# Optimization experiments

Hardware: AMD Instinct MI355X
Metric: run time of the kernel (lower is better)

Reference implementation:

```python
import jax, jax.numpy as jnp
import numpy as np

N = 100000
E = 3200000
D = 128
H = 128
BN_EPS = 1e-5


def setup_inputs() -> dict:
    key = jax.random.key(0)
    ks = jax.random.split(key, 8)
    x = jax.random.normal(ks[0], (N, D), dtype=jnp.float32)
    edge_index = jax.random.randint(ks[1], (2, E), 0, N, dtype=jnp.int64)
    edge_attr = jax.random.normal(ks[2], (E, 1), dtype=jnp.float32)
    # MLP params (Linear stores weight [out,in]; we keep [in,out] for x @ W)
    W1 = jax.random.normal(ks[3], (D, H), dtype=jnp.float32) / np.sqrt(D)
    b1 = jnp.zeros((H,), dtype=jnp.float32)
    W2 = jax.random.normal(ks[4], (H, H), dtype=jnp.float32) / np.sqrt(H)
    b2 = jnp.zeros((H,), dtype=jnp.float32)
    gamma = jnp.ones((H,), dtype=jnp.float32)
    beta = jnp.zeros((H,), dtype=jnp.float32)
    return {"x": x, "edge_index": edge_index, "edge_attr": edge_attr,
            "W1": W1, "b1": b1, "W2": W2, "b2": b2,
            "gamma": gamma, "beta": beta}


def reference(x, edge_index, edge_attr, W1, b1, W2, b2, gamma, beta):
    src, dst = edge_index[0], edge_index[1]
    # GIN aggregation: (1 + eps) * x_i + sum_{j->i} x_j, eps = 0
    agg = jax.ops.segment_sum(x[src], dst, num_segments=N)  # [N, D]
    h = x + agg
    # 2-layer MLP
    h = jax.nn.relu(h @ W1 + b1)
    h = h @ W2 + b2
    # outer ReLU
    h = jax.nn.relu(h)
    # BatchNorm1d (training mode: batch stats, biased variance)
    mean = jnp.mean(h, axis=0)
    var = jnp.mean(jnp.square(h - mean), axis=0)
    h = (h - mean) * jax.lax.rsqrt(var + BN_EPS) * gamma + beta
    return h
```

## Files before the change

kernel.cpp:

```cpp
#include <hip/hip_runtime.h>

#define N_NODES 100000
#define DIM 128
#define PT_TILE 4096
#define PT_THR 512

#define NPB1 196
#define NB1 511
#define CAP1 7168
#define NPB2 256
#define NB2 391
#define CAP2 12288

typedef unsigned int u32;
typedef unsigned short u16;
typedef __attribute__((ext_vector_type(8))) short bf16x8;
typedef __attribute__((ext_vector_type(4))) float f32x4;

__device__ __forceinline__ float bf16_to_f(u16 v) {
  return __uint_as_float(((u32)v) << 16);
}
__device__ __forceinline__ u16 f_to_bf16(float f) {
  u32 b = __float_as_uint(f);
  b += 0x7fff + ((b >> 16) & 1);
  return (u16)(b >> 16);
}
__device__ __forceinline__ float blo(u32 q) { return __uint_as_float(q << 16); }
__device__ __forceinline__ float bhi(u32 q) {
  return __uint_as_float(q & 0xffff0000u);
}
__device__ __forceinline__ u32 packbf(float lo, float hi) {
  return ((u32)f_to_bf16(hi) << 16) | (u32)f_to_bf16(lo);
}

__global__ __launch_bounds__(256) void prep1_kernel(
    const float* __restrict__ W1, u16* __restrict__ Wt1,
    const float* __restrict__ W2, u16* __restrict__ Wt2,
    int* __restrict__ gcur, float* __restrict__ stats) {
  int blk = blockIdx.x;
  if (blk < 64) {
    int id = blk * 256 + threadIdx.x;
    Wt1[id] = f_to_bf16(W1[(id & 127) * DIM + (id >> 7)]);
  } else if (blk < 128) {
    int id = (blk - 64) * 256 + threadIdx.x;
    Wt2[id] = f_to_bf16(W2[(id & 127) * DIM + (id >> 7)]);
  } else if (blk == 128) {
    for (int i = threadIdx.x; i < NB1; i += 256) gcur[i] = i * CAP1;
  } else {
    for (int i = threadIdx.x; i < 768; i += 256) stats[i] = 0.f;
  }
}

__global__ __launch_bounds__(256) void prep2_kernel(
    const float* __restrict__ W1, u16* __restrict__ Wt1,
    const float* __restrict__ W2, u16* __restrict__ Wt2,
    const int* __restrict__ ei, int* __restrict__ bcnt, int E_) {
  int blk = blockIdx.x;
  if (blk < 64) {
    int id = blk * 256 + threadIdx.x;
    Wt1[id] = f_to_bf16(W1[(id & 127) * DIM + (id >> 7)]);
  } else if (blk < 128) {
    int id = (blk - 64) * 256 + threadIdx.x;
    Wt2[id] = f_to_bf16(W2[(id & 127) * DIM + (id >> 7)]);
  } else {
    __shared__ int lc[NB2];
    for (int i = threadIdx.x; i < NB2; i += 256) lc[i] = 0;
    __syncthreads();
    const int* dst = ei + E_;
    int G = 512 * 256;
    int g = (blk - 128) * 256 + threadIdx.x;
    int n4 = E_ >> 2;
    const int4* d4 = (const int4*)dst;
    for (int i = g; i < n4; i += G) {
      int4 v = d4[i];
      atomicAdd(&lc[((u32)v.x) >> 8], 1);
      atomicAdd(&lc[((u32)v.y) >> 8], 1);
      atomicAdd(&lc[((u32)v.z) >> 8], 1);
      atomicAdd(&lc[((u32)v.w) >> 8], 1);
    }
    for (int e = (n4 << 2) + g; e < E_; e += G)
      atomicAdd(&lc[((u32)dst[e]) >> 8], 1);
    __syncthreads();
    for (int i = threadIdx.x; i < NB2; i += 256)
      if (lc[i]) atomicAdd(&bcnt[i], lc[i]);
  }
}

__global__ void bscan_kernel(const int* __restrict__ bcnt,
                             int* __restrict__ boffs, int* __restrict__ gcur) {
  __shared__ int s[256];
  int t = threadIdx.x;
  int v0 = (2 * t < NB2) ? bcnt[2 * t] : 0;
  int v1 = (2 * t + 1 < NB2) ? bcnt[2 * t + 1] : 0;
  int ts = v0 + v1;
  s[t] = ts;
  __syncthreads();
  for (int o = 1; o < 256; o <<= 1) {
    int u = (t >= o) ? s[t - o] : 0;
    __syncthreads();
    s[t] += u;
    __syncthreads();
  }
  int excl = s[t] - ts;
  if (2 * t <= NB2) boffs[2 * t] = excl;
  if (2 * t + 1 <= NB2) boffs[2 * t + 1] = excl + v0;
  if (2 * t < NB2) gcur[2 * t] = excl;
  if (2 * t + 1 < NB2) gcur[2 * t + 1] = excl + v0;
}

template <int NPB, int NBU>
__global__ __launch_bounds__(PT_THR) void part_cvt_kernel(
    const int* __restrict__ ei, int* __restrict__ gcur,
    u32* __restrict__ packed, int E_, const float* __restrict__ x,
    u16* __restrict__ xb) {
  __shared__ u32 keys[PT_TILE];
  __shared__ u16 bid[PT_TILE];
  __shared__ int lh[NBU];
  __shared__ int lpos[NBU];
  __shared__ int gpos[NBU];
  __shared__ int ss[PT_THR];
  const int nPart = (E_ + PT_TILE - 1) / PT_TILE;
  const int t = threadIdx.x;

  if (blockIdx.x >= nPart) {
    int cb = blockIdx.x - nPart;
    int total = N_NODES * DIM / 4;
    int stride = 1024 * PT_THR;
    for (int i = cb * PT_THR + t; i < total; i += stride) {
      float4 v = reinterpret_cast<const float4*>(x)[i];
      ushort4 o;
      o.x = f_to_bf16(v.x);
      o.y = f_to_bf16(v.y);
      o.z = f_to_bf16(v.z);
      o.w = f_to_bf16(v.w);
      reinterpret_cast<ushort4*>(xb)[i] = o;
    }
    return;
  }

  const int base = blockIdx.x * PT_TILE;
  const int cnt = min(PT_TILE, E_ - base);

  for (int i = t; i < NBU; i += PT_THR) lh[i] = 0;
  __syncthreads();

  u32 pk[8];
  int bb[8];
#pragma unroll
  for (int k = 0; k < 8; ++k) {
    int e = base + k * PT_THR + t;
    if (k * PT_THR + t < cnt) {
      int src = ei[e];
      u32 dst = (u32)ei[E_ + e];
      u32 b = dst / NPB;
      bb[k] = (int)b;
      pk[k] = (u32)src | ((dst - b * NPB) << 17);
      atomicAdd(&lh[bb[k]], 1);
    } else {
      bb[k] = -1;
    }
  }
  __syncthreads();

  int v = (t < NBU) ? lh[t] : 0;
  ss[t] = v;
  __syncthreads();
  for (int o = 1; o < PT_THR; o <<= 1) {
    int u = (t >= o) ? ss[t - o] : 0;
    __syncthreads();
    ss[t] += u;
    __syncthreads();
  }
  if (t < NBU) {
    lpos[t] = ss[t] - v;
    if (v > 0) gpos[t] = atomicAdd(&gcur[t], v);
  }
  __syncthreads();

#pragma unroll
  for (int k = 0; k < 8; ++k) {
    if (bb[k] >= 0) {
      int p = atomicAdd(&lpos[bb[k]], 1);
      keys[p] = pk[k];
      bid[p] = (u16)bb[k];
    }
  }
  __syncthreads();

  for (int i = t; i < cnt; i += PT_THR) {
    int b = bid[i];
    int startb = lpos[b] - lh[b];
    packed[gpos[b] + (i - startb)] = keys[i];
  }
}

template <int NPB, int LCAP, bool FIXED>
__global__ __launch_bounds__(1024) void sortgather_kernel(
    const u32* __restrict__ packed, const int* __restrict__ boffs,
    const int* __restrict__ gcur, const uint4* __restrict__ xb4,
    uint4* __restrict__ hb4) {
  __shared__ u32 sorted_[LCAP];
  __shared__ int hist[256], cur[256], ssc[256];
  __shared__ int nodeoff[257];
  const int b = blockIdx.x;
  const int t = threadIdx.x;
  int base, cnt;
  if (FIXED) {
    base = b * LCAP;
    cnt = gcur[b] - base;
  } else {
    base = boffs[b];
    cnt = boffs[b + 1] - base;
  }
  if (cnt > LCAP) cnt = LCAP;
  if (cnt < 0) cnt = 0;

  if (t < 256) hist[t] = 0;
  __syncthreads();
  for (int i = t; i < cnt; i += 1024)
    atomicAdd(&hist[packed[base + i] >> 17], 1);
  __syncthreads();
  if (t < 256) ssc[t] = hist[t];
  __syncthreads();
  for (int o = 1; o < 256; o <<= 1) {
    int u = 0;
    if (t < 256 && t >= o) u = ssc[t - o];
    __syncthreads();
    if (t < 256) ssc[t] += u;
    __syncthreads();
  }
  if (t < 256) {
    int excl = ssc[t] - hist[t];
    cur[t] = excl;
    nodeoff[t] = excl;
  }
  if (t == 0) nodeoff[256] = cnt;
  __syncthreads();
  for (int i = t; i < cnt; i += 1024) {
    u32 v = packed[base + i];
    int p = atomicAdd(&cur[v >> 17], 1);
    sorted_[p] = v & 0x1FFFFu;
  }
  __syncthreads();

  const int wv = t >> 6;
  const int lane = t & 63;
  const int g = lane >> 4;
  const int l = lane & 15;
  constexpr int K = (NPB + 15) / 16;
#pragma unroll 1
  for (int k = 0; k < K; ++k) {
    int nl = wv + (k << 4);
    if (nl >= NPB) break;
    int n = b * NPB + nl;
    if (n >= N_NODES) break;
    int beg = nodeoff[nl], end = nodeoff[nl + 1];
    float a0 = 0.f, a1 = 0.f, a2 = 0.f, a3 = 0.f;
    float a4 = 0.f, a5 = 0.f, a6 = 0.f, a7 = 0.f;
    if (g == 0) {
      uint4 q = xb4[(size_t)n * 16 + l];
      a0 = blo(q.x); a1 = bhi(q.x);
      a2 = blo(q.y); a3 = bhi(q.y);
      a4 = blo(q.z); a5 = bhi(q.z);
      a6 = blo(q.w); a7 = bhi(q.w);
    }
    int j = beg + g;
    for (; j + 12 < end; j += 16) {
      int s0 = sorted_[j], s1 = sorted_[j + 4];
      int s2 = sorted_[j + 8], s3 = sorted_[j + 12];
      uint4 q0 = xb4[(size_t)s0 * 16 + l];
      uint4 q1 = xb4[(size_t)s1 * 16 + l];
      uint4 q2 = xb4[(size_t)s2 * 16 + l];
      uint4 q3 = xb4[(size_t)s3 * 16 + l];
      a0 += blo(q0.x); a1 += bhi(q0.x);
      a2 += blo(q0.y); a3 += bhi(q0.y);
      a4 += blo(q0.z); a5 += bhi(q0.z);
      a6 += blo(q0.w); a7 += bhi(q0.w);
      a0 += blo(q1.x); a1 += bhi(q1.x);
      a2 += blo(q1.y); a3 += bhi(q1.y);
      a4 += blo(q1.z); a5 += bhi(q1.z);
      a6 += blo(q1.w); a7 += bhi(q1.w);
      a0 += blo(q2.x); a1 += bhi(q2.x);
      a2 += blo(q2.y); a3 += bhi(q2.y);
      a4 += blo(q2.z); a5 += bhi(q2.z);
      a6 += blo(q2.w); a7 += bhi(q2.w);
      a0 += blo(q3.x); a1 += bhi(q3.x);
      a2 += blo(q3.y); a3 += bhi(q3.y);
      a4 += blo(q3.z); a5 += bhi(q3.z);
      a6 += blo(q3.w); a7 += bhi(q3.w);
    }
    for (; j < end; j += 4) {
      uint4 q = xb4[(size_t)sorted_[j] * 16 + l];
      a0 += blo(q.x); a1 += bhi(q.x);
      a2 += blo(q.y); a3 += bhi(q.y);
      a4 += blo(q.z); a5 += bhi(q.z);
      a6 += blo(q.w); a7 += bhi(q.w);
    }
    a0 += __shfl_xor(a0, 16); a1 += __shfl_xor(a1, 16);
    a2 += __shfl_xor(a2, 16); a3 += __shfl_xor(a3, 16);
    a4 += __shfl_xor(a4, 16); a5 += __shfl_xor(a5, 16);
    a6 += __shfl_xor(a6, 16); a7 += __shfl_xor(a7, 16);
    a0 += __shfl_xor(a0, 32); a1 += __shfl_xor(a1, 32);
    a2 += __shfl_xor(a2, 32); a3 += __shfl_xor(a3, 32);
    a4 += __shfl_xor(a4, 32); a5 += __shfl_xor(a5, 32);
    a6 += __shfl_xor(a6, 32); a7 += __shfl_xor(a7, 32);
    if (g == 0) {
      uint4 o;
      o.x = packbf(a0, a1);
      o.y = packbf(a2, a3);
      o.z = packbf(a4, a5);
      o.w = packbf(a6, a7);
      hb4[(size_t)n * 16 + l] = o;
    }
  }
}

__global__ __launch_bounds__(256) void mlp_mfma_kernel(
    u16* __restrict__ hb, const u16* __restrict__ Wt1,
    const u16* __restrict__ Wt2, const float* __restrict__ b1,
    const float* __restrict__ b2, float* __restrict__ pstats) {
  __shared__ u16 sH1[4][16 * DIM];
  __shared__ float sS[4][128], sQ[4][128];
  const int tid = threadIdx.x;
  const int wv = tid >> 6;
  const int lane = tid & 63;
  const int lr = lane & 15;
  const int lq = lane >> 4;
  const int row0 = blockIdx.x * 64 + wv * 16;

  bf16x8 a[4];
  {
    int r = row0 + lr;
    if (r > N_NODES - 1) r = N_NODES - 1;
#pragma unroll
    for (int ks = 0; ks < 4; ++ks)
      a[ks] = *reinterpret_cast<const bf16x8*>(hb + (size_t)r * DIM + ks * 32 +
                                               lq * 8);
  }
  f32x4 acc[8];
#pragma unroll
  for (int ct = 0; ct < 8; ++ct) {
    f32x4 c = {0.f, 0.f, 0.f, 0.f};
#pragma unroll
    for (int ks = 0; ks < 4; ++ks) {
      bf16x8 b = *reinterpret_cast<const bf16x8*>(
          Wt1 + (ct * 16 + lr) * DIM + ks * 32 + lq * 8);
      c = __builtin_amdgcn_mfma_f32_16x16x32_bf16(a[ks], b, c, 0, 0, 0);
    }
    acc[ct] = c;
  }
  char* slab = reinterpret_cast<char*>(&sH1[wv][0]);
#pragma unroll
  for (int ct = 0; ct < 8; ++ct) {
    int c = ct * 16 + lr;
    float bias = b1[c];
#pragma unroll
    for (int j = 0; j < 4; ++j) {
      int rl = lq * 4 + j;
      float y = fmaxf(acc[ct][j] + bias, 0.f);
      int byte = rl * 256 + ((c * 2) ^ ((rl & 7) << 4));
      *reinterpret_cast<u16*>(slab + byte) = f_to_bf16(y);
    }
  }
  __syncthreads();

  bf16x8 a2[4];
#pragma unroll
  for (int ks = 0; ks < 4; ++ks) {
    int byte = lr * 256 + (((ks * 32 + lq * 8) * 2) ^ ((lr & 7) << 4));
    a2[ks] = *reinterpret_cast<const bf16x8*>(slab + byte);
  }
#pragma unroll
  for (int ct = 0; ct < 8; ++ct) {
    f32x4 c = {0.f, 0.f, 0.f, 0.f};
#pragma unroll
    for (int ks = 0; ks < 4; ++ks) {
      bf16x8 b = *reinterpret_cast<const bf16x8*>(
          Wt2 + (ct * 16 + lr) * DIM + ks * 32 + lq * 8);
      c = __builtin_amdgcn_mfma_f32_16x16x32_bf16(a2[ks], b, c, 0, 0, 0);
    }
    acc[ct] = c;
  }
  float ls[8], lss[8];
#pragma unroll
  for (int ct = 0; ct < 8; ++ct) {
    int c = ct * 16 + lr;
    float bias = b2[c];
    ls[ct] = 0.f;
    lss[ct] = 0.f;
#pragma unroll
    for (int j = 0; j < 4; ++j) {
      int r = row0 + lq * 4 + j;
      float y = fmaxf(acc[ct][j] + bias, 0.f);
      u16 yq = f_to_bf16(y);
      float yf = bf16_to_f(yq);
      if (r < N_NODES) {
        hb[(size_t)r * DIM + c] = yq;
        ls[ct] += yf;
        lss[ct] += yf * yf;
      }
    }
  }
#pragma unroll
  for (int ct = 0; ct < 8; ++ct) {
    float s = ls[ct], q = lss[ct];
    s += __shfl_xor(s, 16);
    q += __shfl_xor(q, 16);
    s += __shfl_xor(s, 32);
    q += __shfl_xor(q, 32);
    if (lq == 0) {
      sS[wv][ct * 16 + lr] = s;
      sQ[wv][ct * 16 + lr] = q;
    }
  }
  __syncthreads();
  {
    int t = tid;
    float v;
    if (t < 128)
      v = sS[0][t] + sS[1][t] + sS[2][t] + sS[3][t];
    else
      v = sQ[0][t - 128] + sQ[1][t - 128] + sQ[2][t - 128] + sQ[3][t - 128];
    pstats[(size_t)blockIdx.x * 256 + t] = v;
  }
}

__global__ __launch_bounds__(256) void bn_reduce_kernel(
    const float* __restrict__ pstats, float* __restrict__ stats, int nblk) {
  int t = threadIdx.x;
  float v = 0.f;
  for (int i = blockIdx.x; i < nblk; i += gridDim.x)
    v += pstats[(size_t)i * 256 + t];
  atomicAdd(&stats[t], v);
}

__global__ __launch_bounds__(256) void bn_apply_bf16_kernel(
    const uint4* __restrict__ hb4, const float* __restrict__ stats,
    const float* __restrict__ gamma, const float* __restrict__ beta,
    float4* __restrict__ out4) {
  __shared__ float sSc[128], sSh[128];
  int t = threadIdx.x;
  if (t < 128) {
    float mean = stats[t] / (float)N_NODES;
    float var = stats[128 + t] / (float)N_NODES - mean * mean;
    float scale = gamma[t] * rsqrtf(var + 1e-5f);
    sSc[t] = scale;
    sSh[t] = beta[t] - mean * scale;
  }
  __syncthreads();
  int total = N_NODES * 16;
  int stride = gridDim.x * 256;
  for (int i = blockIdx.x * 256 + t; i < total; i += stride) {
    uint4 q = hb4[i];
    int cb = (i & 15) * 8;
    float4 o0, o1;
    o0.x = blo(q.x) * sSc[cb + 0] + sSh[cb + 0];
    o0.y = bhi(q.x) * sSc[cb + 1] + sSh[cb + 1];
    o0.z = blo(q.y) * sSc[cb + 2] + sSh[cb + 2];
    o0.w = bhi(q.y) * sSc[cb + 3] + sSh[cb + 3];
    o1.x = blo(q.z) * sSc[cb + 4] + sSh[cb + 4];
    o1.y = bhi(q.z) * sSc[cb + 5] + sSh[cb + 5];
    o1.z = blo(q.w) * sSc[cb + 6] + sSh[cb + 6];
    o1.w = bhi(q.w) * sSc[cb + 7] + sSh[cb + 7];
    out4[2 * i] = o0;
    out4[2 * i + 1] = o1;
  }
}

__global__ __launch_bounds__(256) void scatter_kernel(
    const float* __restrict__ x, const int* __restrict__ ei,
    float* __restrict__ h, int E_) {
  long long total = (long long)E_ * 32;
  long long stride = (long long)gridDim.x * blockDim.x;
  for (long long idx = (long long)blockIdx.x * blockDim.x + threadIdx.x;
       idx < total; idx += stride) {
    int e = (int)(idx >> 5);
    int q = (int)(idx & 31);
    float4 v =
        *reinterpret_cast<const float4*>(x + (size_t)ei[e] * DIM + q * 4);
    float* p = h + (size_t)ei[E_ + e] * DIM + q * 4;
    atomicAdd(p + 0, v.x);
    atomicAdd(p + 1, v.y);
    atomicAdd(p + 2, v.z);
    atomicAdd(p + 3, v.w);
  }
}

__global__ __launch_bounds__(256) void add_x_kernel(const float* __restrict__ x,
                                                    float* __restrict__ h) {
  size_t total = (size_t)N_NODES * DIM / 4;
  size_t stride = (size_t)gridDim.x * blockDim.x;
  for (size_t i = (size_t)blockIdx.x * blockDim.x + threadIdx.x; i < total;
       i += stride) {
    float4 v = reinterpret_cast<float4*>(h)[i];
    float4 xv = reinterpret_cast<const float4*>(x)[i];
    v.x += xv.x; v.y += xv.y; v.z += xv.z; v.w += xv.w;
    reinterpret_cast<float4*>(h)[i] = v;
  }
}

__global__ __launch_bounds__(256) void mlp_valu_kernel(
    float* hbuf, const float* __restrict__ W1, const float* __restrict__ b1,
    const float* __restrict__ W2, const float* __restrict__ b2) {
  __shared__ float sW[DIM * DIM];
  __shared__ float sH[32][DIM];
  const int tid = threadIdx.x;
  const int col = tid & 127;
  const int rhalf = tid >> 7;
  const int row0 = blockIdx.x * 32;

  for (int i = tid; i < DIM * DIM; i += 256) sW[i] = W1[i];
  for (int i = tid; i < 32 * DIM; i += 256) {
    int r = i >> 7, c = i & 127;
    sH[r][c] = hbuf[(size_t)(row0 + r) * DIM + c];
  }
  __syncthreads();
  float acc[16];
  float bias = b1[col];
#pragma unroll
  for (int j = 0; j < 16; ++j) acc[j] = bias;
#pragma unroll 4
  for (int k = 0; k < DIM; ++k) {
    float w = sW[k * DIM + col];
#pragma unroll
    for (int j = 0; j < 16; ++j) acc[j] = fmaf(sH[2 * j + rhalf][k], w, acc[j]);
  }
  __syncthreads();
  for (int i = tid; i < DIM * DIM; i += 256) sW[i] = W2[i];
#pragma unroll
  for (int j = 0; j < 16; ++j) sH[2 * j + rhalf][col] = fmaxf(acc[j], 0.f);
  __syncthreads();
  float bias2 = b2[col];
#pragma unroll
  for (int j = 0; j < 16; ++j) acc[j] = bias2;
#pragma unroll 4
  for (int k = 0; k < DIM; ++k) {
    float w = sW[k * DIM + col];
#pragma unroll
    for (int j = 0; j < 16; ++j) acc[j] = fmaf(sH[2 * j + rhalf][k], w, acc[j]);
  }
#pragma unroll
  for (int j = 0; j < 16; ++j)
    hbuf[(size_t)(row0 + 2 * j + rhalf) * DIM + col] = fmaxf(acc[j], 0.f);
}

__global__ __launch_bounds__(256) void bn_stats_kernel(
    const float* __restrict__ h, float* __restrict__ stats) {
  int col = threadIdx.x & 127;
  int rsub = threadIdx.x >> 7;
  int rstep = gridDim.x * 2;
  float s = 0.f, ss = 0.f;
  for (int r = blockIdx.x * 2 + rsub; r < N_NODES; r += rstep) {
    float v = h[(size_t)r * DIM + col];
    s += v;
    ss += v * v;
  }
  __shared__ float ls[256], lss[256];
  ls[threadIdx.x] = s;
  lss[threadIdx.x] = ss;
  __syncthreads();
  if (threadIdx.x < 128) {
    atomicAdd(&stats[col], ls[threadIdx.x] + ls[threadIdx.x + 128]);
    atomicAdd(&stats[DIM + col], lss[threadIdx.x] + lss[threadIdx.x + 128]);
  }
}

__global__ void bn_scale_kernel(const float* __restrict__ stats,
                                const float* __restrict__ gamma,
                                const float* __restrict__ beta,
                                float* __restrict__ sc) {
  int c = threadIdx.x;
  float mean = stats[c] / (float)N_NODES;
  float var = stats[DIM + c] / (float)N_NODES - mean * mean;
  float scale = gamma[c] * rsqrtf(var + 1e-5f);
  sc[c] = scale;
  sc[DIM + c] = beta[c] - mean * scale;
}

__global__ __launch_bounds__(256) void bn_apply_kernel(
    float* __restrict__ h, const float* __restrict__ sc) {
  size_t total = (size_t)N_NODES * DIM / 4;
  size_t stride = (size_t)gridDim.x * blockDim.x;
  for (size_t i = (size_t)blockIdx.x * blockDim.x + threadIdx.x; i < total;
       i += stride) {
    float4 v = reinterpret_cast<float4*>(h)[i];
    int c = (int)((i * 4) & 127);
    v.x = v.x * sc[c + 0] + sc[DIM + c + 0];
    v.y = v.y * sc[c + 1] + sc[DIM + c + 1];
    v.z = v.z * sc[c + 2] + sc[DIM + c + 2];
    v.w = v.w * sc[c + 3] + sc[DIM + c + 3];
    reinterpret_cast<float4*>(h)[i] = v;
  }
}

extern "C" void kernel_launch(void* const* d_in, const int* in_sizes, int n_in,
                              void* d_out, int out_size, void* d_ws,
                              size_t ws_size, hipStream_t stream) {
  const float* x = (const float*)d_in[0];
  const int* ei = (const int*)d_in[1];
  const float* W1 = (const float*)d_in[3];
  const float* b1 = (const float*)d_in[4];
  const float* W2 = (const float*)d_in[5];
  const float* b2 = (const float*)d_in[6];
  const float* gamma = (const float*)d_in[7];
  const float* beta = (const float*)d_in[8];
  float* out = (float*)d_out;
  int E_ = in_sizes[1] / 2;

  const size_t XB_B = (size_t)N_NODES * DIM * 2;
  char* w = (char*)d_ws;

  size_t o1 = 0;
  u16* t1_xb = (u16*)(w + o1); o1 += XB_B;
  u16* t1_hb = (u16*)(w + o1); o1 += XB_B;
  u16* t1_Wt1 = (u16*)(w + o1); o1 += 32768;
  u16* t1_Wt2 = (u16*)(w + o1); o1 += 32768;
  u32* t1_packed = (u32*)(w + o1);
  o1 += ((size_t)NB1 * CAP1 + 8192) * 4;
  float* t1_stats = (float*)(w + o1); o1 += 3072;
  int* t1_gcur = (int*)(w + o1); o1 += 2560;
  size_t need1 = o1;

  size_t o2 = 0;
  u16* t2_xb = (u16*)(w + o2); o2 += XB_B;
  u16* t2_hb = (u16*)(w + o2); o2 += XB_B;
  u16* t2_Wt1 = (u16*)(w + o2); o2 += 32768;
  u16* t2_Wt2 = (u16*)(w + o2); o2 += 32768;
  u32* t2_packed = (u32*)(w + o2); o2 += (size_t)E_ * 4;
  int* t2_bcnt = (int*)(w + o2); o2 += 1600;
  float* t2_stats = (float*)(w + o2); o2 += 3072;
  int* t2_boffs = (int*)(w + o2); o2 += 1600;
  int* t2_gcur = (int*)(w + o2); o2 += 1600;
  size_t need2 = o2;

  const int nPartBlocks = (E_ + PT_TILE - 1) / PT_TILE;
  const int nMlpBlocks = (N_NODES + 63) / 64;

  if (ws_size >= need1) {
    float* pstats = (float*)t1_xb;
    prep1_kernel<<<130, 256, 0, stream>>>(W1, t1_Wt1, W2, t1_Wt2, t1_gcur,
                                          t1_stats);
    part_cvt_kernel<NPB1, NB1><<<nPartBlocks + 1024, PT_THR, 0, stream>>>(
        ei, t1_gcur, t1_packed, E_, x, t1_xb);
    sortgather_kernel<NPB1, CAP1, true><<<NB1, 1024, 0, stream>>>(
        t1_packed, nullptr, t1_gcur, (const uint4*)t1_xb, (uint4*)t1_hb);
    mlp_mfma_kernel<<<nMlpBlocks, 256, 0, stream>>>(t1_hb, t1_Wt1, t1_Wt2, b1,
                                                    b2, pstats);
    bn_reduce_kernel<<<32, 256, 0, stream>>>(pstats, t1_stats, nMlpBlocks);
    bn_apply_bf16_kernel<<<2048, 256, 0, stream>>>(
        (const uint4*)t1_hb, t1_stats, gamma, beta, (float4*)out);
  } else if (ws_size >= need2) {
    float* pstats = (float*)t2_xb;
    hipMemsetAsync(t2_bcnt, 0, 1600 + 3072, stream);
    prep2_kernel<<<640, 256, 0, stream>>>(W1, t2_Wt1, W2, t2_Wt2, ei, t2_bcnt,
                                          E_);
    bscan_kernel<<<1, 256, 0, stream>>>(t2_bcnt, t2_boffs, t2_gcur);
    part_cvt_kernel<NPB2, NB2><<<nPartBlocks + 1024, PT_THR, 0, stream>>>(
        ei, t2_gcur, t2_packed, E_, x, t2_xb);
    sortgather_kernel<NPB2, CAP2, false><<<NB2, 1024, 0, stream>>>(
        t2_packed, t2_boffs, nullptr, (const uint4*)t2_xb, (uint4*)t2_hb);
    mlp_mfma_kernel<<<nMlpBlocks, 256, 0, stream>>>(t2_hb, t2_Wt1, t2_Wt2, b1,
                                                    b2, pstats);
    bn_reduce_kernel<<<32, 256, 0, stream>>>(pstats, t2_stats, nMlpBlocks);
    bn_apply_bf16_kernel<<<2048, 256, 0, stream>>>(
        (const uint4*)t2_hb, t2_stats, gamma, beta, (float4*)out);
  } else {
    float* s2 = (float*)d_ws;
    hipMemsetAsync(out, 0, (size_t)N_NODES * DIM * sizeof(float), stream);
    hipMemsetAsync(s2, 0, 768 * sizeof(float), stream);
    scatter_kernel<<<4096, 256, 0, stream>>>(x, ei, out, E_);
    add_x_kernel<<<2048, 256, 0, stream>>>(x, out);
    mlp_valu_kernel<<<(N_NODES + 31) / 32, 256, 0, stream>>>(out, W1, b1, W2,
                                                             b2);
    bn_stats_kernel<<<1024, 256, 0, stream>>>(out, s2);
    bn_scale_kernel<<<1, 128, 0, stream>>>(s2, gamma, beta, s2 + 256);
    bn_apply_kernel<<<2048, 256, 0, stream>>>(out, s2 + 256);
  }
}
```

Measured before the change: 247.2 us.

## Scatter partitioned edges directly to global memory and double partition tile size

The partition kernel no longer stages keys in shared memory with a block-wide scan. Each edge now writes straight to its bucket's global slot, found from the global offset plus a per-bucket shared atomic counter. The tile grows to 8192 edges per block, with 16 edges per thread. This removes the scan barriers and the shared staging pass and halves the number of global atomics per bucket. The cost is less coalesced global writes and more registers per thread. Also, nPart changes, so the conversion-block indexing that depends on it and any host grid sizing must stay consistent.

```diff
diff --git a/kernel.cpp b/kernel.cpp
--- a/kernel.cpp
+++ b/kernel.cpp
@@ -2,7 +2,7 @@
 
 #define N_NODES 100000
 #define DIM 128
-#define PT_TILE 4096
+#define PT_TILE 8192
 #define PT_THR 512
 
 #define NPB1 196
@@ -113,12 +113,9 @@
     const int* __restrict__ ei, int* __restrict__ gcur,
     u32* __restrict__ packed, int E_, const float* __restrict__ x,
     u16* __restrict__ xb) {
-  __shared__ u32 keys[PT_TILE];
-  __shared__ u16 bid[PT_TILE];
   __shared__ int lh[NBU];
   __shared__ int lpos[NBU];
   __shared__ int gpos[NBU];
-  __shared__ int ss[PT_THR];
   const int nPart = (E_ + PT_TILE - 1) / PT_TILE;
   const int t = threadIdx.x;
 
@@ -144,10 +141,10 @@
   for (int i = t; i < NBU; i += PT_THR) lh[i] = 0;
   __syncthreads();
 
-  u32 pk[8];
-  int bb[8];
-#pragma unroll
-  for (int k = 0; k < 8; ++k) {
+  u32 pk[16];
+  int bb[16];
+#pragma unroll
+  for (int k = 0; k < 16; ++k) {
     int e = base + k * PT_THR + t;
     if (k * PT_THR + t < cnt) {
       int src = ei[e];
@@ -162,35 +159,19 @@
   }
   __syncthreads();
 
-  int v = (t < NBU) ? lh[t] : 0;
-  ss[t] = v;
-  __syncthreads();
-  for (int o = 1; o < PT_THR; o <<= 1) {
-    int u = (t >= o) ? ss[t - o] : 0;
-    __syncthreads();
-    ss[t] += u;
-    __syncthreads();
-  }
-  if (t < NBU) {
-    lpos[t] = ss[t] - v;
-    if (v > 0) gpos[t] = atomicAdd(&gcur[t], v);
-  }
-  __syncthreads();
-
-#pragma unroll
-  for (int k = 0; k < 8; ++k) {
+  for (int i = t; i < NBU; i += PT_THR) {
+    int v = lh[i];
+    if (v > 0) gpos[i] = atomicAdd(&gcur[i], v);
+    lpos[i] = 0;
+  }
+  __syncthreads();
+
+#pragma unroll
+  for (int k = 0; k < 16; ++k) {
     if (bb[k] >= 0) {
-      int p = atomicAdd(&lpos[bb[k]], 1);
-      keys[p] = pk[k];
-      bid[p] = (u16)bb[k];
-    }
-  }
-  __syncthreads();
-
-  for (int i = t; i < cnt; i += PT_THR) {
-    int b = bid[i];
-    int startb = lpos[b] - lh[b];
-    packed[gpos[b] + (i - startb)] = keys[i];
+      int p = gpos[bb[k]] + atomicAdd(&lpos[bb[k]], 1);
+      packed[p] = pk[k];
+    }
   }
 }
 
```

Measured after the change: 253.2 us. 1.02x slower.
